# Kernel tuning notes

Measured on AMD Instinct MI355X. Metric: run time of the kernel, lower is better.

The kernel has to match this reference:

```python
import jax, jax.numpy as jnp
import numpy as np
from jax.scipy.special import gammaln, logsumexp

T, K, D = 262144, 32, 64


def setup_inputs() -> dict:
    key = jax.random.key(0)
    ks = jax.random.split(key, 7)
    Y = jax.random.normal(ks[0], (T, D), dtype=jnp.float32)
    dT = jax.random.uniform(ks[1], (T,), dtype=jnp.float32) + 0.01  # strictly positive intervals
    A = jax.random.normal(ks[2], (K, K), dtype=jnp.float32)
    log_ab = jax.random.normal(ks[3], (K, 2), dtype=jnp.float32) * 0.5
    mu = jax.random.normal(ks[4], (K, D), dtype=jnp.float32)
    log_sigma = jax.random.normal(ks[5], (K, D), dtype=jnp.float32) * 0.1
    pi = jax.random.normal(ks[6], (K,), dtype=jnp.float32)
    return {"Y": Y, "dT": dT, "A": A, "log_ab": log_ab, "mu": mu, "log_sigma": log_sigma, "pi": pi}


def _gamma_ll(dT, log_ab):
    # per-state Gamma(concentration=exp(log_ab[:,0]), rate=exp(log_ab[:,1])) log_prob -> [T, K]
    a = jnp.exp(log_ab[:, 0])
    b = jnp.exp(log_ab[:, 1])
    const = a * log_ab[:, 1] - gammaln(a)  # a*log(b) - lgamma(a)
    return const[None, :] + jnp.log(dT)[:, None] * (a - 1.0)[None, :] - dT[:, None] * b[None, :]


def _gauss_ll(Y, mu, log_sigma):
    # diagonal-Gaussian emission log-likelihood summed over D, via GEMMs -> [T, K]
    inv_var = jnp.exp(-2.0 * log_sigma)  # [K, D]
    quad = (-0.5) * (Y * Y) @ inv_var.T + Y @ (mu * inv_var).T - 0.5 * jnp.sum(mu * mu * inv_var, axis=-1)[None, :]
    const = -jnp.sum(log_sigma, axis=-1) - 0.5 * D * jnp.log(2.0 * jnp.pi).astype(Y.dtype)
    return quad + const[None, :]


def _hmm_lognorm(pi0, logA, ll):
    # log-domain forward algorithm; returns log normalizer (scalar)
    alpha0 = pi0 + ll[0]

    def step(alpha, ll_t):
        # alpha_t[j] = logsumexp_i(alpha[i] + logA[i, j]) + ll_t[j]
        alpha = logsumexp(alpha[:, None] + logA, axis=0) + ll_t
        return alpha, None

    alphaT, _ = jax.lax.scan(step, alpha0, ll[1:])
    return logsumexp(alphaT)


def reference(Y, dT, A, log_ab, mu, log_sigma, pi):
    h = Y  # obs_model embedding (identity for Gaussian emission model)
    y_ll = _gauss_ll(Y, mu, log_sigma)          # [T, K]
    y_loss = jnp.zeros((), dtype=Y.dtype)
    dT_ll = _gamma_ll(dT, log_ab)               # [T, K]
    ll = y_ll + dT_ll
    logA = jax.nn.log_softmax(A, axis=1)        # LogSoftmax(dim=1)(A)
    pi0 = jax.nn.log_softmax(pi, axis=0)        # LogSoftmax(dim=0)(pi)
    loss = -1.0 * _hmm_lognorm(pi0, logA, ll) + y_loss
    return h, loss
```

## Files before the change

### kernel.cpp

```cpp
#include <hip/hip_runtime.h>
#include <stdint.h>

#define TT 262144
#define KK 32
#define DD 64
#define LSTEP 32
#define PCH 8192

typedef __attribute__((ext_vector_type(4)))  float f4v;
typedef __attribute__((ext_vector_type(16))) float f16v;
typedef __attribute__((ext_vector_type(4)))  short s4v;
typedef __attribute__((ext_vector_type(2)))  int   i2v;
typedef __attribute__((ext_vector_type(2)))  unsigned int u2v;
typedef __attribute__((ext_vector_type(4)))  unsigned int u4v;

#define WS_AFRAG_US 0
#define WS_WFRAG_US 1024
#define WS_WF    2560
#define WS_CK    6656
#define WS_AM1   6688
#define WS_BB    6720
#define WS_PI0   6752
#define WS_LS    8192
#define WS_LS2   16384
#define SH_MATS  33280
#define SH_MATS2 (33280 + PCH*1024)
#define LN2F 0.69314718055994531f

__device__ __forceinline__ unsigned pkbf(float hi, float lo) {
    return __builtin_amdgcn_perm(__builtin_bit_cast(unsigned, hi),
                                 __builtin_bit_cast(unsigned, lo), 0x07060302u);
}
__device__ __forceinline__ unsigned short f2bf_rne(float f) {
    unsigned u = __builtin_bit_cast(unsigned, f);
    unsigned r = u + 0x7FFFu + ((u >> 16) & 1u);
    return (unsigned short)(r >> 16);
}
__device__ __forceinline__ float bf2f(unsigned short u) {
    return __builtin_bit_cast(float, (unsigned)u << 16);
}
__device__ __forceinline__ float wmax32(float v) {
    v = fmaxf(v, __shfl_xor(v, 1));  v = fmaxf(v, __shfl_xor(v, 2));
    v = fmaxf(v, __shfl_xor(v, 4));  v = fmaxf(v, __shfl_xor(v, 8));
    v = fmaxf(v, __shfl_xor(v, 16));
    return v;
}
__device__ __forceinline__ float wmax64(float v) {
    v = wmax32(v); v = fmaxf(v, __shfl_xor(v, 32));
    return v;
}
__device__ __forceinline__ float wsum32(float v) {
    v += __shfl_xor(v, 1); v += __shfl_xor(v, 2); v += __shfl_xor(v, 4);
    v += __shfl_xor(v, 8); v += __shfl_xor(v, 16);
    return v;
}
__device__ __forceinline__ float wsum64(float v) {
    v = wsum32(v); v += __shfl_xor(v, 32);
    return v;
}
__device__ __forceinline__ float wval(int dd, int k, const float* mu, const float* lsg) {
    int d = dd & 63;
    float lv = lsg[k * DD + d];
    float iv = __expf(-2.f * lv);
    return (dd < DD) ? (-0.5f * iv) : (mu[k * DD + d] * iv);
}

__global__ void k0_prep(const float* __restrict__ Y, const float* __restrict__ A,
                        const float* __restrict__ lab, const float* __restrict__ mu,
                        const float* __restrict__ lsg, const float* __restrict__ pi,
                        float* __restrict__ ws, float* __restrict__ out)
{
    __shared__ float lseA[KK];
    const int tid = threadIdx.x;
    if (tid < KK) {
        float m = -1e30f;
        for (int j = 0; j < KK; ++j) m = fmaxf(m, A[tid * KK + j]);
        float s = 0.f;
        for (int j = 0; j < KK; ++j) s += __expf(A[tid * KK + j] - m);
        lseA[tid] = m + __logf(s);

        float mp = -1e30f;
        for (int j = 0; j < KK; ++j) mp = fmaxf(mp, pi[j]);
        float sp = 0.f;
        for (int j = 0; j < KK; ++j) sp += __expf(pi[j] - mp);
        ws[WS_PI0 + tid] = pi[tid] - (mp + __logf(sp));

        float la = lab[tid * 2 + 0], lb = lab[tid * 2 + 1];
        float a = __expf(la), b = __expf(lb);
        float c1 = 0.f, c2 = 0.f;
        for (int d = 0; d < DD; ++d) {
            float lv = lsg[tid * DD + d];
            float mv = mu[tid * DD + d];
            c1 -= lv;
            c2 += mv * mv * __expf(-2.f * lv);
        }
        ws[WS_CK + tid]  = a * lb - lgammaf(a) + c1 - 0.5f * c2 - 32.f * 1.8378770664093453f;
        ws[WS_AM1 + tid] = a - 1.f;
        ws[WS_BB + tid]  = b;
    }
    __syncthreads();
    unsigned short* us = (unsigned short*)ws;
    for (int idx = tid; idx < 1024; idx += 256) {
        int g = idx >> 8, rem = idx & 255, ln = rem >> 2, e = rem & 3;
        int m = 8 * g + 4 * (ln >> 5) + e, i = ln & 31;
        us[WS_AFRAG_US + idx] = f2bf_rne(__expf(A[m * KK + i] - lseA[m]));
    }
    for (int idx = tid; idx < 4096; idx += 256) {
        int s = idx >> 8, rem = idx & 255, ln = rem >> 2, e = rem & 3;
        int dd = 8 * s + 4 * (ln >> 5) + e, k = ln & 31;
        us[WS_WFRAG_US + idx] = f2bf_rne(wval(dd, k, mu, lsg));
    }
    for (int idx = tid; idx < 4096; idx += 256) {
        int dd = idx >> 5, k = idx & 31;
        ws[WS_WF + idx] = wval(dd, k, mu, lsg);
    }
    if (tid < DD) out[tid] = Y[tid];
}

__global__ __launch_bounds__(256, 6) void k1_scan(
    const float* __restrict__ Y, const float* __restrict__ dTp,
    float* __restrict__ ws, float* __restrict__ out)
{
    __shared__ __align__(16) float E[4][32][32];
    __shared__ __align__(16) float dtv[4][32], dtl[4][32];

    const int tid = threadIdx.x;
    const int wv = tid >> 6, l = tid & 63, h = l >> 5, c = l & 31;
    const int p = blockIdx.x * 4 + wv;
    const int t0 = 1 + p * LSTEP;
    const int nsteps = min(LSTEP, TT - t0);

    const unsigned short* afr = (const unsigned short*)ws + WS_AFRAG_US;
    const unsigned short* wfr = (const unsigned short*)ws + WS_WFRAG_US;

    const float cK = ws[WS_CK + c], am1 = ws[WS_AM1 + c], bb = ws[WS_BB + c];

    if (l < 32) {
        int t = t0 + l;
        float dv = (t < TT) ? dTp[t] : 1.f;
        dtv[wv][l] = dv;
        dtl[wv][l] = __logf(dv);
    }

    f16v zf;
    #pragma unroll
    for (int r = 0; r < 16; ++r) zf[r] = 0.f;

    f16v acc = zf;
    s4v rawf[8];
    const int trow = t0 + c;
    const bool vld = trow < TT;
    const float* yrow = Y + (size_t)trow * DD;
    float* orow = out + (size_t)trow * DD;
    #pragma unroll
    for (int g = 0; g < 8; ++g) {
        const int col = 8 * g + 4 * h;
        f4v y4; y4[0] = 0.f; y4[1] = 0.f; y4[2] = 0.f; y4[3] = 0.f;
        if (vld) y4 = *(const f4v*)(yrow + col);
        if (vld) *(f4v*)(orow + col) = y4;
        f4v q4 = y4 * y4;
        i2v sq; sq[0] = pkbf(q4[1], q4[0]); sq[1] = pkbf(q4[3], q4[2]);
        i2v rw; rw[0] = pkbf(y4[1], y4[0]); rw[1] = pkbf(y4[3], y4[2]);
        rawf[g] = __builtin_bit_cast(s4v, rw);
        s4v wf = *(const s4v*)(wfr + g * 256 + l * 4);
        acc = __builtin_amdgcn_mfma_f32_32x32x8bf16_1k(__builtin_bit_cast(s4v, sq), wf, acc, 0, 0, 0);
    }
    #pragma unroll
    for (int g = 0; g < 8; ++g) {
        s4v wf = *(const s4v*)(wfr + (8 + g) * 256 + l * 4);
        acc = __builtin_amdgcn_mfma_f32_32x32x8bf16_1k(rawf[g], wf, acc, 0, 0, 0);
    }

    s4v aF[4];
    #pragma unroll
    for (int g = 0; g < 4; ++g) aF[g] = *(const s4v*)(afr + g * 256 + l * 4);

    asm volatile("s_waitcnt lgkmcnt(0)" ::: "memory");

    float csv = 0.f;
    #pragma unroll
    for (int m = 0; m < 4; ++m) {
        const f4v dv4 = *(const f4v*)(&dtv[wv][8 * m + 4 * h]);
        const f4v dl4 = *(const f4v*)(&dtl[wv][8 * m + 4 * h]);
        #pragma unroll
        for (int j = 0; j < 4; ++j) {
            const int row = 8 * m + 4 * h + j;
            float llv = acc[4 * m + j] + cK + am1 * dl4[j] - bb * dv4[j];
            float cm = wmax32(llv);
            E[wv][row][c] = __expf(llv - cm);
            csv += (row < nsteps) ? cm : 0.f;
        }
    }
    float cacc = wsum64(csv) * (1.f / 32.f);

    asm volatile("s_waitcnt lgkmcnt(0)" ::: "memory");

    f16v S;
    #pragma unroll
    for (int m = 0; m < 4; ++m)
        #pragma unroll
        for (int j = 0; j < 4; ++j)
            S[4 * m + j] = ((8 * m + 4 * h + j) == c) ? 1.f : 0.f;
    float l2acc = 0.f;

    for (int n = 0; n < nsteps; ++n) {
        f16v Dv = zf;
        #pragma unroll
        for (int g = 0; g < 4; ++g) {
            i2v bd; bd[0] = pkbf(S[4 * g + 1], S[4 * g + 0]);
                    bd[1] = pkbf(S[4 * g + 3], S[4 * g + 2]);
            Dv = __builtin_amdgcn_mfma_f32_32x32x8bf16_1k(aF[g], __builtin_bit_cast(s4v, bd), Dv, 0, 0, 0);
        }
        const f4v* erow = (const f4v*)(&E[wv][n][0]);
        #pragma unroll
        for (int m = 0; m < 4; ++m) {
            const f4v e4 = erow[2 * m + h];
            #pragma unroll
            for (int j = 0; j < 4; ++j) S[4 * m + j] = Dv[4 * m + j] * e4[j];
        }
        if ((n & 3) == 3) {
            float mx = S[0];
            #pragma unroll
            for (int r = 1; r < 16; ++r) mx = fmaxf(mx, S[r]);
            mx = wmax64(mx);
            const float inv = __fdividef(1.f, mx);
            #pragma unroll
            for (int r = 0; r < 16; ++r) S[r] *= inv;
            l2acc += __log2f(mx);
        }
    }

    unsigned short* Tb = (unsigned short*)&E[wv][0][0];
    asm volatile("s_waitcnt lgkmcnt(0)" ::: "memory");
    #pragma unroll
    for (int m = 0; m < 4; ++m)
        #pragma unroll
        for (int j = 0; j < 4; ++j)
            Tb[(8 * m + 4 * h + j) * 36 + c] = f2bf_rne(S[4 * m + j]);
    asm volatile("s_waitcnt lgkmcnt(0)" ::: "memory");
    u2v tg[4];
    #pragma unroll
    for (int g = 0; g < 4; ++g)
        tg[g] = *(const u2v*)(Tb + c * 36 + 8 * g + 4 * h);
    unsigned short* gm = (unsigned short*)ws + SH_MATS + (size_t)p * 1024 + l * 16;
    u4v s0; s0[0] = tg[0][0]; s0[1] = tg[0][1]; s0[2] = tg[1][0]; s0[3] = tg[1][1];
    u4v s1; s1[0] = tg[2][0]; s1[1] = tg[2][1]; s1[2] = tg[3][0]; s1[3] = tg[3][1];
    *(u4v*)(gm) = s0;
    *(u4v*)(gm + 8) = s1;
    if (l == 0) ws[WS_LS + p] = cacc + LN2F * l2acc;
}

__device__ __forceinline__ f16v prodAU(const u4v a0, const u4v a1, const f16v U, const f16v zf) {
    s4v aA[4];
    u2v t;
    t[0] = a0[0]; t[1] = a0[1]; aA[0] = __builtin_bit_cast(s4v, t);
    t[0] = a0[2]; t[1] = a0[3]; aA[1] = __builtin_bit_cast(s4v, t);
    t[0] = a1[0]; t[1] = a1[1]; aA[2] = __builtin_bit_cast(s4v, t);
    t[0] = a1[2]; t[1] = a1[3]; aA[3] = __builtin_bit_cast(s4v, t);
    f16v Dv = zf;
    #pragma unroll
    for (int g = 0; g < 4; ++g) {
        i2v bd; bd[0] = pkbf(U[4 * g + 1], U[4 * g + 0]);
                bd[1] = pkbf(U[4 * g + 3], U[4 * g + 2]);
        Dv = __builtin_amdgcn_mfma_f32_32x32x8bf16_1k(aA[g], __builtin_bit_cast(s4v, bd), Dv, 0, 0, 0);
    }
    return Dv;
}

__global__ __launch_bounds__(128, 1) void k2_combine(float* __restrict__ ws)
{
    __shared__ __align__(16) unsigned short slot[2][1152];
    __shared__ float scl[2], lac[2];
    const int tid = threadIdx.x, wv = tid >> 6, l = tid & 63, h = l >> 5, c = l & 31;
    const int blk = blockIdx.x;
    const int idx0 = blk * 64 + wv * 32;
    const unsigned short* mats = (const unsigned short*)ws + SH_MATS;

    float lsv = (l < 32) ? ws[WS_LS + idx0 + l] : 0.f;
    float lssum = wsum64(lsv);

    f16v zf;
    #pragma unroll
    for (int r = 0; r < 16; ++r) zf[r] = 0.f;
    f16v U;
    #pragma unroll
    for (int m = 0; m < 4; ++m)
        #pragma unroll
        for (int j = 0; j < 4; ++j)
            U[4 * m + j] = ((8 * m + 4 * h + j) == c) ? 1.f : 0.f;
    float l2a = 0.f;

    u4v pf[2][2];
    {
        const u4v* mp0 = (const u4v*)(mats + (size_t)idx0 * 1024) + l * 2;
        const u4v* mp1 = (const u4v*)(mats + (size_t)(idx0 + 1) * 1024) + l * 2;
        pf[0][0] = mp0[0]; pf[0][1] = mp0[1];
        pf[1][0] = mp1[0]; pf[1][1] = mp1[1];
    }
    for (int q = 0; q < 32; ++q) {
        const u4v a0 = pf[q & 1][0], a1 = pf[q & 1][1];
        if (q + 2 < 32) {
            const u4v* mp = (const u4v*)(mats + (size_t)(idx0 + q + 2) * 1024) + l * 2;
            pf[q & 1][0] = mp[0]; pf[q & 1][1] = mp[1];
        }
        f16v Dv = prodAU(a0, a1, U, zf);
        if ((q & 3) == 3) {
            float mx = Dv[0];
            #pragma unroll
            for (int r = 1; r < 16; ++r) mx = fmaxf(mx, Dv[r]);
            mx = wmax64(mx);
            const float inv = __fdividef(1.f, mx);
            #pragma unroll
            for (int r = 0; r < 16; ++r) U[r] = Dv[r] * inv;
            l2a += __log2f(mx);
        } else {
            U = Dv;
        }
    }
    #pragma unroll
    for (int m = 0; m < 4; ++m)
        #pragma unroll
        for (int j = 0; j < 4; ++j)
            slot[wv][(8 * m + 4 * h + j) * 36 + c] = f2bf_rne(U[4 * m + j]);
    if (l == 0) { scl[wv] = lssum; lac[wv] = l2a; }
    __syncthreads();

    if (wv == 0) {
        u4v a0, a1;
        {
            u2v t0 = *(const u2v*)(&slot[1][c * 36 + 0 + 4 * h]);
            u2v t1 = *(const u2v*)(&slot[1][c * 36 + 8 + 4 * h]);
            u2v t2 = *(const u2v*)(&slot[1][c * 36 + 16 + 4 * h]);
            u2v t3 = *(const u2v*)(&slot[1][c * 36 + 24 + 4 * h]);
            a0[0] = t0[0]; a0[1] = t0[1]; a0[2] = t1[0]; a0[3] = t1[1];
            a1[0] = t2[0]; a1[1] = t2[1]; a1[2] = t3[0]; a1[3] = t3[1];
        }
        f16v Dv = prodAU(a0, a1, U, zf);
        float mx = Dv[0];
        #pragma unroll
        for (int r = 1; r < 16; ++r) mx = fmaxf(mx, Dv[r]);
        mx = wmax64(mx);
        const float inv = __fdividef(1.f, mx);
        #pragma unroll
        for (int r = 0; r < 16; ++r) U[r] = Dv[r] * inv;
        const float l2tot = lac[0] + lac[1] + __log2f(mx);
        asm volatile("s_waitcnt lgkmcnt(0)" ::: "memory");
        #pragma unroll
        for (int m = 0; m < 4; ++m)
            #pragma unroll
            for (int j = 0; j < 4; ++j)
                slot[0][(8 * m + 4 * h + j) * 36 + c] = f2bf_rne(U[4 * m + j]);
        asm volatile("s_waitcnt lgkmcnt(0)" ::: "memory");
        u2v tg[4];
        #pragma unroll
        for (int g = 0; g < 4; ++g)
            tg[g] = *(const u2v*)(&slot[0][c * 36 + 8 * g + 4 * h]);
        unsigned short* gm = (unsigned short*)ws + SH_MATS2 + (size_t)blk * 1024 + l * 16;
        u4v s0; s0[0] = tg[0][0]; s0[1] = tg[0][1]; s0[2] = tg[1][0]; s0[3] = tg[1][1];
        u4v s1; s1[0] = tg[2][0]; s1[1] = tg[2][1]; s1[2] = tg[3][0]; s1[3] = tg[3][1];
        *(u4v*)(gm) = s0;
        *(u4v*)(gm + 8) = s1;
        if (l == 0) ws[WS_LS2 + blk] = scl[0] + scl[1] + LN2F * l2tot;
    }
}

__global__ __launch_bounds__(1024, 1) void k3_final(
    const float* __restrict__ Y, const float* __restrict__ dTp,
    float* __restrict__ ws, float* __restrict__ out)
{
    __shared__ __align__(16) unsigned short slot[16][1152];
    __shared__ float sc[16];
    const int tid = threadIdx.x, wv = tid >> 6, l = tid & 63, h = l >> 5, c = l & 31;
    const unsigned short* mats2 = (const unsigned short*)ws + SH_MATS2;

    f16v zf;
    #pragma unroll
    for (int r = 0; r < 16; ++r) zf[r] = 0.f;

    const int idx0 = wv * 8;
    float lsv = (l < 8) ? ws[WS_LS2 + idx0 + l] : 0.f;
    float lssum = wsum64(lsv);
    f16v U;
    #pragma unroll
    for (int m = 0; m < 4; ++m)
        #pragma unroll
        for (int j = 0; j < 4; ++j)
            U[4 * m + j] = ((8 * m + 4 * h + j) == c) ? 1.f : 0.f;
    float l2a = 0.f;
    u4v pf[2][2];
    {
        const u4v* mp0 = (const u4v*)(mats2 + (size_t)idx0 * 1024) + l * 2;
        const u4v* mp1 = (const u4v*)(mats2 + (size_t)(idx0 + 1) * 1024) + l * 2;
        pf[0][0] = mp0[0]; pf[0][1] = mp0[1];
        pf[1][0] = mp1[0]; pf[1][1] = mp1[1];
    }
    for (int q = 0; q < 8; ++q) {
        const u4v a0 = pf[q & 1][0], a1 = pf[q & 1][1];
        if (q + 2 < 8) {
            const u4v* mp = (const u4v*)(mats2 + (size_t)(idx0 + q + 2) * 1024) + l * 2;
            pf[q & 1][0] = mp[0]; pf[q & 1][1] = mp[1];
        }
        f16v Dv = prodAU(a0, a1, U, zf);
        if ((q & 3) == 3) {
            float mx = Dv[0];
            #pragma unroll
            for (int r = 1; r < 16; ++r) mx = fmaxf(mx, Dv[r]);
            mx = wmax64(mx);
            const float inv = __fdividef(1.f, mx);
            #pragma unroll
            for (int r = 0; r < 16; ++r) U[r] = Dv[r] * inv;
            l2a += __log2f(mx);
        } else {
            U = Dv;
        }
    }
    #pragma unroll
    for (int m = 0; m < 4; ++m)
        #pragma unroll
        for (int j = 0; j < 4; ++j)
            slot[wv][(8 * m + 4 * h + j) * 36 + c] = f2bf_rne(U[4 * m + j]);
    if (l == 0) sc[wv] = lssum + LN2F * l2a;
    __syncthreads();

    for (int s = 1; s < 16; s <<= 1) {
        const int cnt = 16 / (2 * s);
        if (wv < cnt) {
            const int i = wv * 2 * s;
            s4v aA[4], bB[4];
            #pragma unroll
            for (int g = 0; g < 4; ++g) {
                u2v t = *(const u2v*)(&slot[i + s][c * 36 + 8 * g + 4 * h]);
                aA[g] = __builtin_bit_cast(s4v, t);
                s4v b;
                #pragma unroll
                for (int j = 0; j < 4; ++j)
                    b[j] = (short)slot[i][(8 * g + 4 * h + j) * 36 + c];
                bB[g] = b;
            }
            f16v Dv = zf;
            #pragma unroll
            for (int g = 0; g < 4; ++g)
                Dv = __builtin_amdgcn_mfma_f32_32x32x8bf16_1k(aA[g], bB[g], Dv, 0, 0, 0);
            float mx = Dv[0];
            #pragma unroll
            for (int r = 1; r < 16; ++r) mx = fmaxf(mx, Dv[r]);
            mx = wmax64(mx);
            const float inv = __fdividef(1.f, mx);
            #pragma unroll
            for (int m = 0; m < 4; ++m)
                #pragma unroll
                for (int j = 0; j < 4; ++j)
                    slot[i][(8 * m + 4 * h + j) * 36 + c] = f2bf_rne(Dv[4 * m + j] * inv);
            if (l == 0) sc[i] = sc[i] + sc[i + s] + __logf(mx);
        }
        __syncthreads();
    }

    if (wv == 0) {
        float acc = 0.f;
        const float* Wf = ws + WS_WF;
        for (int dd = 0; dd < 128; ++dd) {
            const float yv = Y[dd & 63];
            const float f = (dd < 64) ? yv * yv : yv;
            acc = fmaf(f, Wf[dd * 32 + c], acc);
        }
        const float dt0 = dTp[0];
        const float ll0 = acc + ws[WS_CK + c] + ws[WS_AM1 + c] * __logf(dt0) - ws[WS_BB + c] * dt0;
        const float av = ws[WS_PI0 + c] + ll0;
        const float c0 = wmax32(av);
        const float a0 = __expf(av - c0);
        float part = 0.f;
        #pragma unroll
        for (int i = 0; i < 16; ++i) {
            const int ii = 16 * h + i;
            const float m = bf2f(slot[0][c * 36 + ii]);
            const float ai = __shfl(a0, ii);
            part = fmaf(m, ai, part);
        }
        const float srow = part + __shfl_xor(part, 32);
        const float tot = wsum32(srow);
        if (l == 0) out[(size_t)TT * DD] = -(sc[0] + c0 + __logf(tot));
    }
}

extern "C" void kernel_launch(void* const* d_in, const int* in_sizes, int n_in,
                              void* d_out, int out_size, void* d_ws, size_t ws_size,
                              hipStream_t stream)
{
    const float* Y   = (const float*)d_in[0];
    const float* dTp = (const float*)d_in[1];
    const float* A   = (const float*)d_in[2];
    const float* lab = (const float*)d_in[3];
    const float* mu  = (const float*)d_in[4];
    const float* lsg = (const float*)d_in[5];
    const float* pi  = (const float*)d_in[6];
    float* out = (float*)d_out;
    float* ws  = (float*)d_ws;

    hipLaunchKernelGGL(k0_prep, dim3(1), dim3(256), 0, stream, Y, A, lab, mu, lsg, pi, ws, out);
    hipLaunchKernelGGL(k1_scan, dim3(PCH / 4), dim3(256), 0, stream, Y, dTp, ws, out);
    hipLaunchKernelGGL(k2_combine, dim3(128), dim3(128), 0, stream, ws);
    hipLaunchKernelGGL(k3_final, dim3(1), dim3(1024), 0, stream, Y, dTp, ws, out);
}
```

Measured before the change: 213.7 us.

## Coalesce Y loads via LDS staging and fully unroll the scan loop

Y rows are now loaded with contiguous, coalesced float4 accesses into a padded LDS tile, copied to the output, and then read back transposed for the MFMA fragments. Before, each lane read a strided row segment. The same LDS buffer is reused for the exp-likelihood matrix, and the 32-step recurrence is fully unrolled for every chunk except the last. Launch bounds drop from 6 to 4 waves per SIMD to make room for the larger LDS tile and the extra registers from unrolling. The cost is lower occupancy and more LDS traffic.

```diff
diff --git a/kernel.cpp b/kernel.cpp
--- a/kernel.cpp
+++ b/kernel.cpp
@@ -6,6 +6,7 @@
 #define DD 64
 #define LSTEP 32
 #define PCH 8192
+#define YSTRIDE 68
 
 typedef __attribute__((ext_vector_type(4)))  float f4v;
 typedef __attribute__((ext_vector_type(16))) float f16v;
@@ -117,11 +118,11 @@
     if (tid < DD) out[tid] = Y[tid];
 }
 
-__global__ __launch_bounds__(256, 6) void k1_scan(
+__global__ __launch_bounds__(256, 4) void k1_scan(
     const float* __restrict__ Y, const float* __restrict__ dTp,
     float* __restrict__ ws, float* __restrict__ out)
 {
-    __shared__ __align__(16) float E[4][32][32];
+    __shared__ __align__(16) float Yt[4][32 * YSTRIDE];
     __shared__ __align__(16) float dtv[4][32], dtl[4][32];
 
     const int tid = threadIdx.x;
@@ -146,19 +147,27 @@
     #pragma unroll
     for (int r = 0; r < 16; ++r) zf[r] = 0.f;
 
+    {
+        const size_t gbase = (size_t)t0 * DD;
+        const int r = (l >> 4);
+        const int col = (l & 15) * 4;
+        #pragma unroll
+        for (int i = 0; i < 8; ++i) {
+            const size_t gi = gbase + (size_t)i * 256 + l * 4;
+            f4v y4; y4[0] = 0.f; y4[1] = 0.f; y4[2] = 0.f; y4[3] = 0.f;
+            const bool ok = gi < (size_t)TT * DD;
+            if (ok) y4 = *(const f4v*)(Y + gi);
+            if (ok) *(f4v*)(out + gi) = y4;
+            *(f4v*)(&Yt[wv][(i * 4 + r) * YSTRIDE + col]) = y4;
+        }
+    }
+
     f16v acc = zf;
     s4v rawf[8];
-    const int trow = t0 + c;
-    const bool vld = trow < TT;
-    const float* yrow = Y + (size_t)trow * DD;
-    float* orow = out + (size_t)trow * DD;
     #pragma unroll
     for (int g = 0; g < 8; ++g) {
-        const int col = 8 * g + 4 * h;
-        f4v y4; y4[0] = 0.f; y4[1] = 0.f; y4[2] = 0.f; y4[3] = 0.f;
-        if (vld) y4 = *(const f4v*)(yrow + col);
-        if (vld) *(f4v*)(orow + col) = y4;
-        f4v q4 = y4 * y4;
+        const f4v y4 = *(const f4v*)(&Yt[wv][c * YSTRIDE + 8 * g + 4 * h]);
+        const f4v q4 = y4 * y4;
         i2v sq; sq[0] = pkbf(q4[1], q4[0]); sq[1] = pkbf(q4[3], q4[2]);
         i2v rw; rw[0] = pkbf(y4[1], y4[0]); rw[1] = pkbf(y4[3], y4[2]);
         rawf[g] = __builtin_bit_cast(s4v, rw);
@@ -175,8 +184,6 @@
     #pragma unroll
     for (int g = 0; g < 4; ++g) aF[g] = *(const s4v*)(afr + g * 256 + l * 4);
 
-    asm volatile("s_waitcnt lgkmcnt(0)" ::: "memory");
-
     float csv = 0.f;
     #pragma unroll
     for (int m = 0; m < 4; ++m) {
@@ -187,7 +194,7 @@
             const int row = 8 * m + 4 * h + j;
             float llv = acc[4 * m + j] + cK + am1 * dl4[j] - bb * dv4[j];
             float cm = wmax32(llv);
-            E[wv][row][c] = __expf(llv - cm);
+            Yt[wv][row * YSTRIDE + c] = __expf(llv - cm);
             csv += (row < nsteps) ? cm : 0.f;
         }
     }
@@ -203,7 +210,7 @@
             S[4 * m + j] = ((8 * m + 4 * h + j) == c) ? 1.f : 0.f;
     float l2acc = 0.f;
 
-    for (int n = 0; n < nsteps; ++n) {
+    auto step = [&](int n) {
         f16v Dv = zf;
         #pragma unroll
         for (int g = 0; g < 4; ++g) {
@@ -211,26 +218,38 @@
                     bd[1] = pkbf(S[4 * g + 3], S[4 * g + 2]);
             Dv = __builtin_amdgcn_mfma_f32_32x32x8bf16_1k(aF[g], __builtin_bit_cast(s4v, bd), Dv, 0, 0, 0);
         }
-        const f4v* erow = (const f4v*)(&E[wv][n][0]);
         #pragma unroll
         for (int m = 0; m < 4; ++m) {
-            const f4v e4 = erow[2 * m + h];
+            const f4v e4 = *(const f4v*)(&Yt[wv][n * YSTRIDE + 8 * m + 4 * h]);
             #pragma unroll
             for (int j = 0; j < 4; ++j) S[4 * m + j] = Dv[4 * m + j] * e4[j];
         }
-        if ((n & 3) == 3) {
-            float mx = S[0];
-            #pragma unroll
-            for (int r = 1; r < 16; ++r) mx = fmaxf(mx, S[r]);
-            mx = wmax64(mx);
-            const float inv = __fdividef(1.f, mx);
-            #pragma unroll
-            for (int r = 0; r < 16; ++r) S[r] *= inv;
-            l2acc += __log2f(mx);
-        }
-    }
-
-    unsigned short* Tb = (unsigned short*)&E[wv][0][0];
+    };
+    auto rescale = [&]() {
+        float mx = S[0];
+        #pragma unroll
+        for (int r = 1; r < 16; ++r) mx = fmaxf(mx, S[r]);
+        mx = wmax64(mx);
+        const float inv = __fdividef(1.f, mx);
+        #pragma unroll
+        for (int r = 0; r < 16; ++r) S[r] *= inv;
+        l2acc += __log2f(mx);
+    };
+
+    if (p != PCH - 1) {
+        #pragma unroll
+        for (int n = 0; n < LSTEP; ++n) {
+            step(n);
+            if ((n & 3) == 3) rescale();
+        }
+    } else {
+        for (int n = 0; n < nsteps; ++n) {
+            step(n);
+            if ((n & 3) == 3) rescale();
+        }
+    }
+
+    unsigned short* Tb = (unsigned short*)&Yt[wv][0];
     asm volatile("s_waitcnt lgkmcnt(0)" ::: "memory");
     #pragma unroll
     for (int m = 0; m < 4; ++m)
```

Result: faster. 189.1 us (-11.5%).
